# Optimization experiments

Hardware: AMD Instinct MI355X
Metric: run time of the kernel (lower is better)

Reference implementation:

```python
import jax, jax.numpy as jnp
import numpy as np

B, T, U, V = 8, 128, 64, 512
BLANK = 0
NEG_INF = -1e30  # finite 'log zero' to keep gradients NaN-free


def setup_inputs() -> dict:
    key = jax.random.key(0)
    k1, k2, k3, k4, k5 = jax.random.split(key, 5)
    emissions = jax.random.normal(k1, (B, T, V), dtype=jnp.float32)
    predictions = jax.random.normal(k2, (B, U, V), dtype=jnp.float32)
    labels = jax.random.randint(k3, (B, U - 1), 1, V, dtype=jnp.int32)
    # max(input_lengths) must equal T; max(label_lengths) must equal U-1
    input_lengths = jax.random.randint(k4, (B,), T // 2, T + 1, dtype=jnp.int32).at[0].set(T)
    label_lengths = jax.random.randint(k5, (B,), (U - 1) // 2, U, dtype=jnp.int32).at[0].set(U - 1)
    return {
        "emissions": emissions,
        "predictions": predictions,
        "labels": labels,
        "input_lengths": input_lengths,
        "label_lengths": label_lengths,
    }


def _rnnt_costs(emissions, predictions, labels, input_lengths, label_lengths, blank=BLANK):
    b, t_len, v = emissions.shape
    u_len = predictions.shape[1]
    # joint lattice log-probs: log_softmax over vocab of additive joint
    log_probs = jax.nn.log_softmax(
        emissions[:, :, None, :] + predictions[:, None, :, :], axis=-1
    )  # (B, T, U, V)
    blank_lp = log_probs[..., blank]  # (B, T, U)
    lbl = jnp.broadcast_to(labels[:, None, :, None], (b, t_len, u_len - 1, 1))
    label_lp = jnp.take_along_axis(log_probs[:, :, : u_len - 1, :], lbl, axis=3)[..., 0]  # (B,T,U-1)

    def step(a_top, xs):
        # a_top[b,u] = alpha[t-1,u] + blank_lp[t-1,u]  (entry-from-above scores)
        blank_t, label_t = xs  # (B,U), (B,U-1)
        # c[u] = sum_{k<u} label_lp[t,k]  -> alpha[t,u] = c[u] + LSE_{u'<=u}(a_top[u'] - c[u'])
        c = jnp.concatenate(
            [jnp.zeros((b, 1), a_top.dtype), jnp.cumsum(label_t, axis=1)], axis=1
        )  # (B, U)
        alpha_t = c + jax.lax.cumlogsumexp(a_top - c, axis=1)
        a_next = alpha_t + blank_t  # alpha[t,u] + blank_lp[t,u]
        return a_next, a_next

    a0 = jnp.full((b, u_len), NEG_INF, dtype=emissions.dtype).at[:, 0].set(0.0)
    xs = (jnp.moveaxis(blank_lp, 1, 0), jnp.moveaxis(label_lp, 1, 0))
    _, scores = jax.lax.scan(step, a0, xs)  # (T, B, U): alpha[t,u]+blank_lp[t,u]
    scores = jnp.moveaxis(scores, 1, 0)  # (B, T, U)
    bidx = jnp.arange(b)
    # cost_b = -(alpha[T_b-1, U_b] + blank_lp[T_b-1, U_b])
    costs = -scores[bidx, input_lengths - 1, label_lengths]
    return costs


def reference(emissions, predictions, labels, input_lengths, label_lengths):
    return _rnnt_costs(emissions, predictions, labels, input_lengths, label_lengths)
```

## Files before the change

### kernel.cpp

```cpp
#include <hip/hip_runtime.h>

#define B 8
#define T 128
#define U 64
#define V 512
#define LN2 0.6931471805599453f

template<int CTRL, int ROWM>
__device__ __forceinline__ float dpp_movf(float x, int old_bits) {
    int r = __builtin_amdgcn_update_dpp(old_bits, __builtin_bit_cast(int, x),
                                        CTRL, ROWM, 0xF, false);
    return __builtin_bit_cast(float, r);
}
__device__ __forceinline__ float wave_sum63(float x) {
    x += dpp_movf<0x111, 0xF>(x, 0);
    x += dpp_movf<0x112, 0xF>(x, 0);
    x += dpp_movf<0x114, 0xF>(x, 0);
    x += dpp_movf<0x118, 0xF>(x, 0);
    x += dpp_movf<0x142, 0xA>(x, 0);
    x += dpp_movf<0x143, 0xC>(x, 0);
    return x;
}
__device__ __forceinline__ float wave_max63(float x) {
    const int NI = (int)0xff800000u;
    x = fmaxf(x, dpp_movf<0x111, 0xF>(x, NI));
    x = fmaxf(x, dpp_movf<0x112, 0xF>(x, NI));
    x = fmaxf(x, dpp_movf<0x114, 0xF>(x, NI));
    x = fmaxf(x, dpp_movf<0x118, 0xF>(x, NI));
    x = fmaxf(x, dpp_movf<0x142, 0xA>(x, NI));
    x = fmaxf(x, dpp_movf<0x143, 0xC>(x, NI));
    return x;
}
__device__ __forceinline__ float rdlane(float x, int lane) {
    return __builtin_bit_cast(float,
        __builtin_amdgcn_readlane(__builtin_bit_cast(int, x), lane));
}
__device__ __forceinline__ float dpp_shr1(float x) {
    int r = __builtin_amdgcn_update_dpp(0, __builtin_bit_cast(int, x),
                                        0x138, 0xF, 0xF, false);
    return __builtin_bit_cast(float, r);
}

__global__ __launch_bounds__(256) void lp_kernel(
    const float* __restrict__ em, const float* __restrict__ pr,
    const int* __restrict__ labels,
    float* __restrict__ blankP, float* __restrict__ labelP)
{
    __shared__ float Pexp[32][V];

    const int bid  = blockIdx.x;
    const int ug   = bid & 1;
    const int tg   = (bid >> 1) & 15;
    const int b    = bid >> 5;
    const int lane = threadIdx.x & 63;
    const int wave = threadIdx.x >> 6;

    #pragma unroll 2
    for (int r = 0; r < 8; ++r) {
        const int ul = wave * 8 + r;
        const int gu = ug * 32 + ul;
        const float* prow = pr + ((size_t)b * U + gu) * V;
        const float4 xa = ((const float4*)prow)[lane];
        const float4 xb = ((const float4*)prow)[64 + lane];
        float m = fmaxf(fmaxf(fmaxf(xa.x, xa.y), fmaxf(xa.z, xa.w)),
                        fmaxf(fmaxf(xb.x, xb.y), fmaxf(xb.z, xb.w)));
        const float mp = rdlane(wave_max63(m), 63);
        float4 oa, ob;
        oa.x = __expf(xa.x - mp); oa.y = __expf(xa.y - mp);
        oa.z = __expf(xa.z - mp); oa.w = __expf(xa.w - mp);
        ob.x = __expf(xb.x - mp); ob.y = __expf(xb.y - mp);
        ob.z = __expf(xb.z - mp); ob.w = __expf(xb.w - mp);
        ((float4*)&Pexp[ul][0])[lane]      = oa;
        ((float4*)&Pexp[ul][0])[64 + lane] = ob;
    }
    __syncthreads();

    const int t0 = tg * 8 + wave * 2;
    const int t1 = t0 + 1;
    const float* er0 = em + ((size_t)b * T + t0) * V;
    const float* er1 = em + ((size_t)b * T + t1) * V;
    const float4 ea0 = ((const float4*)er0)[lane];
    const float4 eb0 = ((const float4*)er0)[64 + lane];
    const float4 ea1 = ((const float4*)er1)[lane];
    const float4 eb1 = ((const float4*)er1)[64 + lane];
    float m0 = fmaxf(fmaxf(fmaxf(ea0.x, ea0.y), fmaxf(ea0.z, ea0.w)),
                     fmaxf(fmaxf(eb0.x, eb0.y), fmaxf(eb0.z, eb0.w)));
    float m1 = fmaxf(fmaxf(fmaxf(ea1.x, ea1.y), fmaxf(ea1.z, ea1.w)),
                     fmaxf(fmaxf(eb1.x, eb1.y), fmaxf(eb1.z, eb1.w)));
    const float me0 = rdlane(wave_max63(m0), 63);
    const float me1 = rdlane(wave_max63(m1), 63);
    float E0[8], E1[8];
    E0[0] = __expf(ea0.x - me0); E0[1] = __expf(ea0.y - me0);
    E0[2] = __expf(ea0.z - me0); E0[3] = __expf(ea0.w - me0);
    E0[4] = __expf(eb0.x - me0); E0[5] = __expf(eb0.y - me0);
    E0[6] = __expf(eb0.z - me0); E0[7] = __expf(eb0.w - me0);
    E1[0] = __expf(ea1.x - me1); E1[1] = __expf(ea1.y - me1);
    E1[2] = __expf(ea1.z - me1); E1[3] = __expf(ea1.w - me1);
    E1[4] = __expf(eb1.x - me1); E1[5] = __expf(eb1.y - me1);
    E1[6] = __expf(eb1.z - me1); E1[7] = __expf(eb1.w - me1);

    float S0 = 1.0f, S1 = 1.0f;
    #pragma unroll 2
    for (int ul = 0; ul < 32; ++ul) {
        const float4 pa = ((const float4*)&Pexp[ul][0])[lane];
        const float4 pb = ((const float4*)&Pexp[ul][0])[64 + lane];
        float p0 = E0[0] * pa.x;
        p0 = fmaf(E0[1], pa.y, p0); p0 = fmaf(E0[2], pa.z, p0);
        p0 = fmaf(E0[3], pa.w, p0); p0 = fmaf(E0[4], pb.x, p0);
        p0 = fmaf(E0[5], pb.y, p0); p0 = fmaf(E0[6], pb.z, p0);
        p0 = fmaf(E0[7], pb.w, p0);
        float p1 = E1[0] * pa.x;
        p1 = fmaf(E1[1], pa.y, p1); p1 = fmaf(E1[2], pa.z, p1);
        p1 = fmaf(E1[3], pa.w, p1); p1 = fmaf(E1[4], pb.x, p1);
        p1 = fmaf(E1[5], pb.y, p1); p1 = fmaf(E1[6], pb.z, p1);
        p1 = fmaf(E1[7], pb.w, p1);
        const float s0 = rdlane(wave_sum63(p0), 63);
        const float s1 = rdlane(wave_sum63(p1), 63);
        if (lane == ul) { S0 = s0; S1 = s1; }
    }

    if (lane < 32) {
        const int gu = ug * 32 + lane;
        const float Ppb = Pexp[lane][0];
        const float r0 = 1.0f / S0, r1 = 1.0f / S1;
        const float ebl0 = __expf(er0[0] - me0);
        const float ebl1 = __expf(er1[0] - me1);
        const size_t o0 = ((size_t)b * T + t0) * U + gu;
        const size_t o1 = o0 + U;
        blankP[o0] = ebl0 * Ppb * r0;
        blankP[o1] = ebl1 * Ppb * r1;
        if (gu < U - 1) {
            const int lb = labels[b * (U - 1) + gu];
            const float Ppl = Pexp[lane][lb];
            labelP[o0] = __expf(er0[lb] - me0) * Ppl * r0;
            labelP[o1] = __expf(er1[lb] - me1) * Ppl * r1;
        }
    }
}

__global__ __launch_bounds__(256) void alpha_kernel(
    const float* __restrict__ blankP, const float* __restrict__ labelP,
    const int* __restrict__ in_len, const int* __restrict__ lab_len,
    float* __restrict__ out)
{
    __shared__ float blankQ[(T + 2) * U];
    __shared__ float labelQ[T * U];

    const int b   = blockIdx.x;
    const int tid = threadIdx.x;

    const float* gb = blankP + (size_t)b * T * U;
    const float* gl = labelP + (size_t)b * T * U;
    float4* sb = (float4*)(blankQ + U);
    const float4* gb4 = (const float4*)gb;
    for (int i = tid; i < (T * U) / 4; i += 256) sb[i] = gb4[i];
    if (tid < 2 * U) {
        const int r = (tid < U) ? 0 : (T + 1);
        blankQ[r * U + (tid & (U - 1))] = 0.0f;
    }
    for (int i = tid; i < T * U; i += 256)
        labelQ[i] = (i & (U - 1)) ? gl[i - 1] : 0.0f;
    __syncthreads();
    if (tid >= 64) return;

    const int u  = tid;
    const int Tb = in_len[b];
    const int Ub = lab_len[b];
    const int dmax = (Tb - 1) + Ub;

    auto ib = [&](int d) {
        int tm = d - 1 - u;
        tm = min(max(tm, -1), T);
        return (tm + 1) * U + u;
    };
    auto il = [&](int d) {
        int tc = d - u;
        tc = min(max(tc, 0), T - 1);
        return tc * U + u;
    };

    float A = (u == 0) ? 1.0f : 0.0f;
    int   off = 0;
    float aCap = 1.0f;
    int   offCap = 0;

    float cb[8], cl[8], nb[8], nl[8];
    #pragma unroll
    for (int j = 0; j < 8; ++j) { cb[j] = blankQ[ib(1 + j)]; cl[j] = labelQ[il(1 + j)]; }

    for (int d0 = 1; d0 <= 185; d0 += 8) {
        #pragma unroll
        for (int j = 0; j < 8; ++j) {
            nb[j] = blankQ[ib(d0 + 8 + j)];
            nl[j] = labelQ[il(d0 + 8 + j)];
            const float left = dpp_shr1(A);
            A = fmaf(A, cb[j], left * cl[j]);
            if ((j & 3) == 3) {
                const float mx = rdlane(wave_max63(A), 63);
                int e = ((__builtin_bit_cast(int, mx) >> 23) & 255) - 127;
                e = max(e, -96);
                A *= __builtin_bit_cast(float, (157 - e) << 23);
                off += e - 30;
            }
            const bool cap = (d0 + j == dmax);
            aCap   = cap ? A   : aCap;
            offCap = cap ? off : offCap;
        }
        #pragma unroll
        for (int j = 0; j < 8; ++j) { cb[j] = nb[j]; cl[j] = nl[j]; }
    }

    if (u == Ub) {
        const float bprob = blankQ[Tb * U + u];
        const float v = __log2f(aCap) + (float)offCap + __log2f(bprob);
        out[b] = -v * LN2;
    }
}

extern "C" void kernel_launch(void* const* d_in, const int* in_sizes, int n_in,
                              void* d_out, int out_size, void* d_ws, size_t ws_size,
                              hipStream_t stream) {
    const float* em      = (const float*)d_in[0];
    const float* pr      = (const float*)d_in[1];
    const int*   labels  = (const int*)d_in[2];
    const int*   in_len  = (const int*)d_in[3];
    const int*   lab_len = (const int*)d_in[4];
    float* out = (float*)d_out;

    float* blankP = (float*)d_ws;
    float* labelP = blankP + (size_t)B * T * U;

    lp_kernel<<<B * T / 4, 256, 0, stream>>>(em, pr, labels, blankP, labelP);
    alpha_kernel<<<B, 256, 0, stream>>>(blankP, labelP, in_len, lab_len, out);
}
```

Measured before the change: 31.57 us.

## Fuse log-prob and alpha kernels using a per-batch atomic completion counter

Merges the two launches into one kernel. Each block writes its blank and label probabilities, fences, and increments a per-batch counter. The first block of each batch then spin-waits until all 32 blocks of that batch have arrived and runs the alpha recursion in place of the old second kernel. This removes one kernel launch and the gap between the two kernels, but adds a hipMemsetAsync call. Correctness now depends on all blocks being co-resident so the spin-wait cannot deadlock.

Measured after the change: 56.40 us. 1.79x slower.

```diff
diff --git a/kernel.cpp b/kernel.cpp
--- a/kernel.cpp
+++ b/kernel.cpp
@@ -41,113 +41,123 @@
     return __builtin_bit_cast(float, r);
 }
 
-__global__ __launch_bounds__(256) void lp_kernel(
+__global__ __launch_bounds__(256) void fused_kernel(
     const float* __restrict__ em, const float* __restrict__ pr,
     const int* __restrict__ labels,
-    float* __restrict__ blankP, float* __restrict__ labelP)
+    const int* __restrict__ in_len, const int* __restrict__ lab_len,
+    float* __restrict__ blankP, float* __restrict__ labelP,
+    unsigned* __restrict__ cnt, float* __restrict__ out)
 {
-    __shared__ float Pexp[32][V];
+    __shared__ __align__(16) float smem[(T + 2) * U + T * U];
 
     const int bid  = blockIdx.x;
     const int ug   = bid & 1;
     const int tg   = (bid >> 1) & 15;
     const int b    = bid >> 5;
-    const int lane = threadIdx.x & 63;
-    const int wave = threadIdx.x >> 6;
-
-    #pragma unroll 2
-    for (int r = 0; r < 8; ++r) {
-        const int ul = wave * 8 + r;
-        const int gu = ug * 32 + ul;
-        const float* prow = pr + ((size_t)b * U + gu) * V;
-        const float4 xa = ((const float4*)prow)[lane];
-        const float4 xb = ((const float4*)prow)[64 + lane];
-        float m = fmaxf(fmaxf(fmaxf(xa.x, xa.y), fmaxf(xa.z, xa.w)),
-                        fmaxf(fmaxf(xb.x, xb.y), fmaxf(xb.z, xb.w)));
-        const float mp = rdlane(wave_max63(m), 63);
-        float4 oa, ob;
-        oa.x = __expf(xa.x - mp); oa.y = __expf(xa.y - mp);
-        oa.z = __expf(xa.z - mp); oa.w = __expf(xa.w - mp);
-        ob.x = __expf(xb.x - mp); ob.y = __expf(xb.y - mp);
-        ob.z = __expf(xb.z - mp); ob.w = __expf(xb.w - mp);
-        ((float4*)&Pexp[ul][0])[lane]      = oa;
-        ((float4*)&Pexp[ul][0])[64 + lane] = ob;
-    }
+    const int tid  = threadIdx.x;
+    const int lane = tid & 63;
+    const int wave = tid >> 6;
+
+    {
+        float (*Pexp)[V] = (float (*)[V])smem;
+
+        #pragma unroll 2
+        for (int r = 0; r < 8; ++r) {
+            const int ul = wave * 8 + r;
+            const int gu = ug * 32 + ul;
+            const float* prow = pr + ((size_t)b * U + gu) * V;
+            const float4 xa = ((const float4*)prow)[lane];
+            const float4 xb = ((const float4*)prow)[64 + lane];
+            float m = fmaxf(fmaxf(fmaxf(xa.x, xa.y), fmaxf(xa.z, xa.w)),
+                            fmaxf(fmaxf(xb.x, xb.y), fmaxf(xb.z, xb.w)));
+            const float mp = rdlane(wave_max63(m), 63);
+            float4 oa, ob;
+            oa.x = __expf(xa.x - mp); oa.y = __expf(xa.y - mp);
+            oa.z = __expf(xa.z - mp); oa.w = __expf(xa.w - mp);
+            ob.x = __expf(xb.x - mp); ob.y = __expf(xb.y - mp);
+            ob.z = __expf(xb.z - mp); ob.w = __expf(xb.w - mp);
+            ((float4*)&Pexp[ul][0])[lane]      = oa;
+            ((float4*)&Pexp[ul][0])[64 + lane] = ob;
+        }
+        __syncthreads();
+
+        const int t0 = tg * 8 + wave * 2;
+        const int t1 = t0 + 1;
+        const float* er0 = em + ((size_t)b * T + t0) * V;
+        const float* er1 = em + ((size_t)b * T + t1) * V;
+        const float4 ea0 = ((const float4*)er0)[lane];
+        const float4 eb0 = ((const float4*)er0)[64 + lane];
+        const float4 ea1 = ((const float4*)er1)[lane];
+        const float4 eb1 = ((const float4*)er1)[64 + lane];
+        float m0 = fmaxf(fmaxf(fmaxf(ea0.x, ea0.y), fmaxf(ea0.z, ea0.w)),
+                         fmaxf(fmaxf(eb0.x, eb0.y), fmaxf(eb0.z, eb0.w)));
+        float m1 = fmaxf(fmaxf(fmaxf(ea1.x, ea1.y), fmaxf(ea1.z, ea1.w)),
+                         fmaxf(fmaxf(eb1.x, eb1.y), fmaxf(eb1.z, eb1.w)));
+        const float me0 = rdlane(wave_max63(m0), 63);
+        const float me1 = rdlane(wave_max63(m1), 63);
+        float E0[8], E1[8];
+        E0[0] = __expf(ea0.x - me0); E0[1] = __expf(ea0.y - me0);
+        E0[2] = __expf(ea0.z - me0); E0[3] = __expf(ea0.w - me0);
+        E0[4] = __expf(eb0.x - me0); E0[5] = __expf(eb0.y - me0);
+        E0[6] = __expf(eb0.z - me0); E0[7] = __expf(eb0.w - me0);
+        E1[0] = __expf(ea1.x - me1); E1[1] = __expf(ea1.y - me1);
+        E1[2] = __expf(ea1.z - me1); E1[3] = __expf(ea1.w - me1);
+        E1[4] = __expf(eb1.x - me1); E1[5] = __expf(eb1.y - me1);
+        E1[6] = __expf(eb1.z - me1); E1[7] = __expf(eb1.w - me1);
+
+        float S0 = 1.0f, S1 = 1.0f;
+        #pragma unroll 2
+        for (int ul = 0; ul < 32; ++ul) {
+            const float4 pa = ((const float4*)&Pexp[ul][0])[lane];
+            const float4 pb = ((const float4*)&Pexp[ul][0])[64 + lane];
+            float p0 = E0[0] * pa.x;
+            p0 = fmaf(E0[1], pa.y, p0); p0 = fmaf(E0[2], pa.z, p0);
+            p0 = fmaf(E0[3], pa.w, p0); p0 = fmaf(E0[4], pb.x, p0);
+            p0 = fmaf(E0[5], pb.y, p0); p0 = fmaf(E0[6], pb.z, p0);
+            p0 = fmaf(E0[7], pb.w, p0);
+            float p1 = E1[0] * pa.x;
+            p1 = fmaf(E1[1], pa.y, p1); p1 = fmaf(E1[2], pa.z, p1);
+            p1 = fmaf(E1[3], pa.w, p1); p1 = fmaf(E1[4], pb.x, p1);
+            p1 = fmaf(E1[5], pb.y, p1); p1 = fmaf(E1[6], pb.z, p1);
+            p1 = fmaf(E1[7], pb.w, p1);
+            const float s0 = rdlane(wave_sum63(p0), 63);
+            const float s1 = rdlane(wave_sum63(p1), 63);
+            if (lane == ul) { S0 = s0; S1 = s1; }
+        }
+
+        if (lane < 32) {
+            const int gu = ug * 32 + lane;
+            const float Ppb = Pexp[lane][0];
+            const float r0 = 1.0f / S0, r1 = 1.0f / S1;
+            const float ebl0 = __expf(er0[0] - me0);
+            const float ebl1 = __expf(er1[0] - me1);
+            const size_t o0 = ((size_t)b * T + t0) * U + gu;
+            const size_t o1 = o0 + U;
+            blankP[o0] = ebl0 * Ppb * r0;
+            blankP[o1] = ebl1 * Ppb * r1;
+            if (gu < U - 1) {
+                const int lb = labels[b * (U - 1) + gu];
+                const float Ppl = Pexp[lane][lb];
+                labelP[o0] = __expf(er0[lb] - me0) * Ppl * r0;
+                labelP[o1] = __expf(er1[lb] - me1) * Ppl * r1;
+            }
+        }
+    }
+
+    __threadfence();
     __syncthreads();
-
-    const int t0 = tg * 8 + wave * 2;
-    const int t1 = t0 + 1;
-    const float* er0 = em + ((size_t)b * T + t0) * V;
-    const float* er1 = em + ((size_t)b * T + t1) * V;
-    const float4 ea0 = ((const float4*)er0)[lane];
-    const float4 eb0 = ((const float4*)er0)[64 + lane];
-    const float4 ea1 = ((const float4*)er1)[lane];
-    const float4 eb1 = ((const float4*)er1)[64 + lane];
-    float m0 = fmaxf(fmaxf(fmaxf(ea0.x, ea0.y), fmaxf(ea0.z, ea0.w)),
-                     fmaxf(fmaxf(eb0.x, eb0.y), fmaxf(eb0.z, eb0.w)));
-    float m1 = fmaxf(fmaxf(fmaxf(ea1.x, ea1.y), fmaxf(ea1.z, ea1.w)),
-                     fmaxf(fmaxf(eb1.x, eb1.y), fmaxf(eb1.z, eb1.w)));
-    const float me0 = rdlane(wave_max63(m0), 63);
-    const float me1 = rdlane(wave_max63(m1), 63);
-    float E0[8], E1[8];
-    E0[0] = __expf(ea0.x - me0); E0[1] = __expf(ea0.y - me0);
-    E0[2] = __expf(ea0.z - me0); E0[3] = __expf(ea0.w - me0);
-    E0[4] = __expf(eb0.x - me0); E0[5] = __expf(eb0.y - me0);
-    E0[6] = __expf(eb0.z - me0); E0[7] = __expf(eb0.w - me0);
-    E1[0] = __expf(ea1.x - me1); E1[1] = __expf(ea1.y - me1);
-    E1[2] = __expf(ea1.z - me1); E1[3] = __expf(ea1.w - me1);
-    E1[4] = __expf(eb1.x - me1); E1[5] = __expf(eb1.y - me1);
-    E1[6] = __expf(eb1.z - me1); E1[7] = __expf(eb1.w - me1);
-
-    float S0 = 1.0f, S1 = 1.0f;
-    #pragma unroll 2
-    for (int ul = 0; ul < 32; ++ul) {
-        const float4 pa = ((const float4*)&Pexp[ul][0])[lane];
-        const float4 pb = ((const float4*)&Pexp[ul][0])[64 + lane];
-        float p0 = E0[0] * pa.x;
-        p0 = fmaf(E0[1], pa.y, p0); p0 = fmaf(E0[2], pa.z, p0);
-        p0 = fmaf(E0[3], pa.w, p0); p0 = fmaf(E0[4], pb.x, p0);
-        p0 = fmaf(E0[5], pb.y, p0); p0 = fmaf(E0[6], pb.z, p0);
-        p0 = fmaf(E0[7], pb.w, p0);
-        float p1 = E1[0] * pa.x;
-        p1 = fmaf(E1[1], pa.y, p1); p1 = fmaf(E1[2], pa.z, p1);
-        p1 = fmaf(E1[3], pa.w, p1); p1 = fmaf(E1[4], pb.x, p1);
-        p1 = fmaf(E1[5], pb.y, p1); p1 = fmaf(E1[6], pb.z, p1);
-        p1 = fmaf(E1[7], pb.w, p1);
-        const float s0 = rdlane(wave_sum63(p0), 63);
-        const float s1 = rdlane(wave_sum63(p1), 63);
-        if (lane == ul) { S0 = s0; S1 = s1; }
-    }
-
-    if (lane < 32) {
-        const int gu = ug * 32 + lane;
-        const float Ppb = Pexp[lane][0];
-        const float r0 = 1.0f / S0, r1 = 1.0f / S1;
-        const float ebl0 = __expf(er0[0] - me0);
-        const float ebl1 = __expf(er1[0] - me1);
-        const size_t o0 = ((size_t)b * T + t0) * U + gu;
-        const size_t o1 = o0 + U;
-        blankP[o0] = ebl0 * Ppb * r0;
-        blankP[o1] = ebl1 * Ppb * r1;
-        if (gu < U - 1) {
-            const int lb = labels[b * (U - 1) + gu];
-            const float Ppl = Pexp[lane][lb];
-            labelP[o0] = __expf(er0[lb] - me0) * Ppl * r0;
-            labelP[o1] = __expf(er1[lb] - me1) * Ppl * r1;
-        }
-    }
-}
-
-__global__ __launch_bounds__(256) void alpha_kernel(
-    const float* __restrict__ blankP, const float* __restrict__ labelP,
-    const int* __restrict__ in_len, const int* __restrict__ lab_len,
-    float* __restrict__ out)
-{
-    __shared__ float blankQ[(T + 2) * U];
-    __shared__ float labelQ[T * U];
-
-    const int b   = blockIdx.x;
-    const int tid = threadIdx.x;
+    if (tid == 0) atomicAdd(&cnt[b], 1u);
+
+    if (tg != 0 || ug != 0) return;
+
+    if (tid == 0) {
+        while (atomicAdd(&cnt[b], 0u) < 32u) __builtin_amdgcn_s_sleep(8);
+        __threadfence();
+    }
+    __syncthreads();
+
+    float* blankQ = smem;
+    float* labelQ = smem + (T + 2) * U;
 
     const float* gb = blankP + (size_t)b * T * U;
     const float* gl = labelP + (size_t)b * T * U;
@@ -227,9 +237,11 @@
     const int*   lab_len = (const int*)d_in[4];
     float* out = (float*)d_out;
 
-    float* blankP = (float*)d_ws;
-    float* labelP = blankP + (size_t)B * T * U;
-
-    lp_kernel<<<B * T / 4, 256, 0, stream>>>(em, pr, labels, blankP, labelP);
-    alpha_kernel<<<B, 256, 0, stream>>>(blankP, labelP, in_len, lab_len, out);
-}
+    float*    blankP = (float*)d_ws;
+    float*    labelP = blankP + (size_t)B * T * U;
+    unsigned* cnt    = (unsigned*)(labelP + (size_t)B * T * U);
+
+    hipMemsetAsync(cnt, 0, B * sizeof(unsigned), stream);
+    fused_kernel<<<B * T / 4, 256, 0, stream>>>(em, pr, labels, in_len, lab_len,
+                                                blankP, labelP, cnt, out);
+}
```
